# Optimization experiments

Measured on AMD Instinct MI355X. Metric: run time of the kernel, lower is better.

## Reference

```python
import jax, jax.numpy as jnp
import numpy as np

WIN_H, WIN_W = 4, 7
WIN = WIN_H * WIN_W  # 28 sample points == feature channels
GRID_OFF = (0.0, 40.0)
SPATIAL_SCALE = 1.0 / 0.4
BN_EPS = 1e-3


def setup_inputs() -> dict:
    key = jax.random.key(0)
    ks = jax.random.split(key, 5)
    B, Cin, H, W = 4, 256, 200, 176
    Cout, N = WIN, 2048
    x = jax.random.normal(ks[0], (B, Cin, H, W), dtype=jnp.float32)
    # boxes [x, y, z, w, l, h, r] in realistic KITTI ranges
    lo = jnp.array([0.0, -40.0, -3.0, 1.5, 3.2, 1.4, -np.pi], jnp.float32)
    hi = jnp.array([70.0, 40.0, 1.0, 2.0, 4.2, 1.8, np.pi], jnp.float32)
    u = jax.random.uniform(ks[1], (B, N, 7), dtype=jnp.float32)
    guided_anchors = lo + u * (hi - lo)
    w1 = jax.random.normal(ks[2], (Cout, Cin, 3, 3), jnp.float32) * 0.02
    gamma = jnp.ones((Cout,), jnp.float32)
    beta = jnp.zeros((Cout,), jnp.float32)
    running_mean = jnp.zeros((Cout,), jnp.float32)
    running_var = jnp.ones((Cout,), jnp.float32)
    w2 = jax.random.normal(ks[3], (Cout, Cout, 1, 1), jnp.float32) * 0.05
    return dict(x=x, guided_anchors=guided_anchors, w1=w1, gamma=gamma,
                beta=beta, running_mean=running_mean, running_var=running_var, w2=w2)


def _convs(x, w1, gamma, beta, mean, var, w2):
    dn = ('NCHW', 'OIHW', 'NCHW')
    y = jax.lax.conv_general_dilated(x, w1, (1, 1), 'SAME', dimension_numbers=dn)
    scale = gamma * jax.lax.rsqrt(var + BN_EPS)
    y = y * scale[:, None, None] + (beta - mean * scale)[:, None, None]  # BN (inference)
    y = jax.nn.relu(y)
    return jax.lax.conv_general_dilated(y, w2, (1, 1), 'SAME', dimension_numbers=dn)


def _gen_sample_grid(box5):
    xg, yg, wg, lg, rg = (box5[:, i] for i in range(5))
    c = jnp.cos(rg)[:, None, None]
    s = jnp.sin(rg)[:, None, None]
    xx = (jnp.linspace(-0.5, 0.5, WIN_H)[None, :] * wg[:, None])[:, :, None]  # (N,4,1)
    yy = (jnp.linspace(-0.5, 0.5, WIN_W)[None, :] * lg[:, None])[:, None, :]  # (N,1,7)
    xpix = xx * c + yy * s + xg[:, None, None]  # (N,4,7)
    ypix = yy * c - xx * s + yg[:, None, None]  # (N,4,7)
    xs = ((jnp.transpose(xpix, (1, 2, 0)) + GRID_OFF[0]) * SPATIAL_SCALE).reshape(WIN, -1)
    ys = ((jnp.transpose(ypix, (1, 2, 0)) + GRID_OFF[1]) * SPATIAL_SCALE).reshape(WIN, -1)
    return xs, ys


def _bilinear_sample(img, xs, ys):
    # img: (C,H,W); xs, ys: (C,N) pixel coords (align_corners=True semantics,
    # zero padding outside) -> (C,N). Channel c samples at grid row c.
    C, H, W = img.shape
    x0 = jnp.floor(xs); y0 = jnp.floor(ys)
    wx = xs - x0; wy = ys - y0
    cidx = jnp.arange(C)[:, None]

    def gather(yf, xf):
        yi = yf.astype(jnp.int32); xi = xf.astype(jnp.int32)
        valid = (yf >= 0) & (yf <= H - 1) & (xf >= 0) & (xf <= W - 1)
        v = img[cidx, jnp.clip(yi, 0, H - 1), jnp.clip(xi, 0, W - 1)]
        return jnp.where(valid, v, 0.0)

    return (gather(y0, x0) * (1 - wx) * (1 - wy)
            + gather(y0, x0 + 1) * wx * (1 - wy)
            + gather(y0 + 1, x0) * (1 - wx) * wy
            + gather(y0 + 1, x0 + 1) * wx * wy)


def reference(x, guided_anchors, w1, gamma, beta, running_mean, running_var, w2):
    feat = _convs(x, w1, gamma, beta, running_mean, running_var, w2)  # (B,28,H,W)
    box5 = guided_anchors[:, :, jnp.array([0, 1, 3, 4, 6])]           # (B,N,5)
    xs, ys = jax.vmap(_gen_sample_grid)(box5)                          # (B,28,N) each
    vals = jax.vmap(_bilinear_sample)(feat, xs, ys)                    # (B,28,N)
    scores = jnp.mean(vals, axis=1)                                    # (B,N)
    return scores.reshape(-1)                                          # (B*N,)
```

## Files before the change

kernel.cpp:

```cpp
#include <hip/hip_runtime.h>
#include <hip/hip_bf16.h>

#define HH 200
#define WW 176
#define CIN 256
#define CO 28
#define BN_EPS 1e-3f

typedef __attribute__((ext_vector_type(8))) short short8;
typedef __attribute__((ext_vector_type(4))) float f32x4;

static __device__ __forceinline__ ushort f2bf(float f) {
    __hip_bfloat16 h = __float2bfloat16(f);
    return __builtin_bit_cast(ushort, h);
}

__global__ void prep_k(const float* __restrict__ w1, const float* __restrict__ gamma,
                       const float* __restrict__ beta, const float* __restrict__ mean,
                       const float* __restrict__ var, ushort* __restrict__ w1b,
                       float* __restrict__ shift)
{
    int idx = blockIdx.x * 256 + threadIdx.x;
    if (idx < CO) {
        float sc = gamma[idx] * rsqrtf(var[idx] + BN_EPS);
        shift[idx] = beta[idx] - mean[idx] * sc;
    }
    if (idx < 9 * 8 * 2 * 64 * 8) {
        int j  = idx & 7;
        int l  = (idx >> 3) & 63;
        int n  = (idx >> 9) & 1;
        int h  = (idx >> 10) & 7;
        int t  = idx >> 13;
        int co = n * 16 + (l & 15);
        int ci = h * 32 + (l >> 4) * 8 + j;
        float v = 0.f;
        if (co < CO) {
            float sc = gamma[co] * rsqrtf(var[co] + BN_EPS);
            v = w1[(co * CIN + ci) * 9 + t] * sc;
        }
        w1b[idx] = f2bf(v);
    }
}

__global__ __launch_bounds__(256, 4) void conv_mfma_k(
    const float* __restrict__ x, const ushort* __restrict__ w1b,
    const float* __restrict__ shift, float* __restrict__ y1)
{
    __shared__ uint4 sbuf[2][180 * 4];

    const int tid  = threadIdx.x;
    const int lane = tid & 63;
    const int w    = tid >> 6;

    const int NB = 11 * 25 * 4;
    const int q = NB / 8, r = NB % 8;
    const int bid  = blockIdx.x;
    const int xcd  = bid & 7;
    const int rank = bid >> 3;
    const int tile = (xcd < r ? xcd * (q + 1) : r * (q + 1) + (xcd - r) * q) + rank;

    const int tx  = tile % 11;
    const int rem = tile / 11;
    const int ty  = rem % 25;
    const int b   = rem / 25;
    const int x0  = tx * 16, y0 = ty * 8;

    const float* xb = x + (size_t)b * CIN * HH * WW;

    int  soff[3]; bool sval[3]; bool sp[3];
#pragma unroll
    for (int it = 0; it < 3; ++it) {
        int p = it * 64 + lane;
        sp[it] = p < 180;
        int rr = p / 18, cc = p - rr * 18;
        int gy = y0 + rr - 1, gx = x0 + cc - 1;
        bool v = (gy >= 0) & (gy < HH) & (gx >= 0) & (gx < WW) & sp[it];
        sval[it] = v;
        soff[it] = v ? gy * WW + gx : 0;
    }

    float pre[3][8];

    auto issue = [&](int h) {
        const float* pl = xb + (size_t)(h * 32 + w * 8) * (HH * WW);
#pragma unroll
        for (int it = 0; it < 3; ++it) {
            if (sp[it]) {
#pragma unroll
                for (int j = 0; j < 8; ++j)
                    pre[it][j] = pl[(size_t)j * (HH * WW) + soff[it]];
            }
        }
    };

    auto wr = [&](int h) {
#pragma unroll
        for (int it = 0; it < 3; ++it) {
            if (sp[it]) {
                int p = it * 64 + lane;
                ushort u[8];
#pragma unroll
                for (int j = 0; j < 8; ++j)
                    u[j] = sval[it] ? f2bf(pre[it][j]) : (ushort)0;
                uint4 val;
                val.x = (uint)u[0] | ((uint)u[1] << 16);
                val.y = (uint)u[2] | ((uint)u[3] << 16);
                val.z = (uint)u[4] | ((uint)u[5] << 16);
                val.w = (uint)u[6] | ((uint)u[7] << 16);
                sbuf[h & 1][p * 4 + ((w + p) & 3)] = val;
            }
        }
    };

    f32x4 acc[2][2];
#pragma unroll
    for (int m = 0; m < 2; ++m)
#pragma unroll
        for (int n = 0; n < 2; ++n)
            acc[m][n] = (f32x4){0.f, 0.f, 0.f, 0.f};

    auto compute = [&](int h) {
        const uint4* sb = sbuf[h & 1];
#pragma unroll
        for (int t = 0; t < 9; ++t) {
            const int dy = t / 3 - 1, dx = t % 3 - 1;
            short8 bfr[2];
#pragma unroll
            for (int n = 0; n < 2; ++n)
                bfr[n] = *(const short8*)(w1b + (size_t)(((t * 8 + h) * 2 + n) * 64 + lane) * 8);
#pragma unroll
            for (int m = 0; m < 2; ++m) {
                int p = (2 * w + m + dy + 1) * 18 + (lane & 15) + dx + 1;
                uint4 av = sb[p * 4 + (((lane >> 4) + p) & 3)];
                short8 af = __builtin_bit_cast(short8, av);
                acc[m][0] = __builtin_amdgcn_mfma_f32_16x16x32_bf16(af, bfr[0], acc[m][0], 0, 0, 0);
                acc[m][1] = __builtin_amdgcn_mfma_f32_16x16x32_bf16(af, bfr[1], acc[m][1], 0, 0, 0);
            }
        }
    };

    issue(0);
    wr(0);
    __syncthreads();

#pragma unroll 1
    for (int h = 0; h < 7; ++h) {
        issue(h + 1);
        compute(h);
        wr(h + 1);
        __syncthreads();
    }
    compute(7);

    const int co0 = lane & 15;
    const int co1 = 16 + co0;
    const float s0 = shift[co0];
    const float s1 = (co1 < CO) ? shift[co1] : 0.f;
#pragma unroll
    for (int m = 0; m < 2; ++m) {
        int gy = y0 + 2 * w + m;
#pragma unroll
        for (int reg = 0; reg < 4; ++reg) {
            int gx = x0 + (lane >> 4) * 4 + reg;
            float* yp = y1 + ((size_t)(b * HH + gy) * WW + gx) * CO;
            float v0 = acc[m][0][reg] + s0;
            yp[co0] = v0 > 0.f ? v0 : 0.f;
            if (co1 < CO) {
                float v1 = acc[m][1][reg] + s1;
                yp[co1] = v1 > 0.f ? v1 : 0.f;
            }
        }
    }
}

__global__ __launch_bounds__(224) void sample_k(
    const float* __restrict__ y1, const float* __restrict__ ga,
    const float* __restrict__ w2, float* __restrict__ out)
{
    __shared__ float red[224];
    const int lb  = threadIdx.x / CO;
    const int k   = threadIdx.x % CO;
    const int box = blockIdx.x * 8 + lb;
    const int b   = box >> 11;

    const float* ap = ga + (size_t)box * 7;
    float xg = ap[0], yg = ap[1], wg = ap[3], lg = ap[4], rg = ap[6];
    float c = cosf(rg), s = sinf(rg);

    const int i = k / 7, j = k % 7;
    float xx = ((float)i * (1.f / 3.f) - 0.5f) * wg;
    float yy = ((float)j * (1.f / 6.f) - 0.5f) * lg;
    float xs = (xx * c + yy * s + xg) * 2.5f;
    float ys = (yy * c - xx * s + yg + 40.f) * 2.5f;

    float x0 = floorf(xs), y0 = floorf(ys);
    float wx = xs - x0,    wy = ys - y0;

    float w2r[CO];
    const float* w2p = w2 + k * CO;
#pragma unroll
    for (int q = 0; q < 7; ++q) {
        float4 t = ((const float4*)w2p)[q];
        w2r[4*q] = t.x; w2r[4*q+1] = t.y; w2r[4*q+2] = t.z; w2r[4*q+3] = t.w;
    }

    float val = 0.f;
    const float* yb = y1 + (size_t)b * HH * WW * CO;
#pragma unroll
    for (int cor = 0; cor < 4; ++cor) {
        float yf = y0 + (float)(cor >> 1);
        float xf = x0 + (float)(cor & 1);
        float cw = ((cor & 1) ? wx : 1.f - wx) * ((cor >> 1) ? wy : 1.f - wy);
        if (yf >= 0.f && yf <= (float)(HH - 1) && xf >= 0.f && xf <= (float)(WW - 1)) {
            int yi = (int)yf, xi = (int)xf;
            const float* p = yb + ((size_t)yi * WW + xi) * CO;
            float d = 0.f;
#pragma unroll
            for (int q = 0; q < 7; ++q) {
                float4 t = ((const float4*)p)[q];
                d = fmaf(w2r[4*q],   t.x, d);
                d = fmaf(w2r[4*q+1], t.y, d);
                d = fmaf(w2r[4*q+2], t.z, d);
                d = fmaf(w2r[4*q+3], t.w, d);
            }
            val = fmaf(cw, d, val);
        }
    }

    red[threadIdx.x] = val;
    __syncthreads();
    if (k == 0) {
        float sum = 0.f;
#pragma unroll
        for (int q = 0; q < CO; ++q) sum += red[lb * CO + q];
        out[box] = sum * (1.f / 28.f);
    }
}

extern "C" void kernel_launch(void* const* d_in, const int* in_sizes, int n_in,
                              void* d_out, int out_size, void* d_ws, size_t ws_size,
                              hipStream_t stream) {
    const float* x     = (const float*)d_in[0];
    const float* ga    = (const float*)d_in[1];
    const float* w1    = (const float*)d_in[2];
    const float* gamma = (const float*)d_in[3];
    const float* beta  = (const float*)d_in[4];
    const float* mean  = (const float*)d_in[5];
    const float* var   = (const float*)d_in[6];
    const float* w2    = (const float*)d_in[7];
    float* out = (float*)d_out;

    ushort* w1b   = (ushort*)d_ws;
    float*  shift = (float*)((char*)d_ws + 147456);
    float*  y1    = (float*)((char*)d_ws + 147968);

    prep_k<<<(9 * 8 * 2 * 64 * 8 + 255) / 256, 256, 0, stream>>>(
        w1, gamma, beta, mean, var, w1b, shift);

    conv_mfma_k<<<11 * 25 * 4, 256, 0, stream>>>(x, w1b, shift, y1);

    sample_k<<<(4 * 2048) / 8, 224, 0, stream>>>(y1, ga, w2, out);
}
```

Baseline: 89.08 us.

## Stage conv weights into LDS via async global_load_lds and single-buffer input tile

Reorders the prepped bf16 weights so each 32-channel chunk is contiguous, then streams each chunk into a double-buffered LDS array with direct global-to-LDS loads instead of reading the B fragments from global memory inside the MFMA loop. To fit the added 36KB of LDS, the input tile becomes single-buffered, which needs an extra barrier per chunk, and the launch-bounds occupancy hint drops from 4 to 3 blocks. The intent is to replace repeated global weight fetches with LDS reads and overlap the weight prefetch with compute, at the cost of more synchronisation and lower occupancy.

After: 76.26 us. -14.4%, faster.

```diff
diff --git a/kernel.cpp b/kernel.cpp
--- a/kernel.cpp
+++ b/kernel.cpp
@@ -14,6 +14,11 @@
     __hip_bfloat16 h = __float2bfloat16(f);
     return __builtin_bit_cast(ushort, h);
 }
+
+#define GLL16(g, l)                                                         \
+    __builtin_amdgcn_global_load_lds(                                       \
+        (const __attribute__((address_space(1))) void*)(g),                 \
+        (__attribute__((address_space(3))) void*)(l), 16, 0, 0)
 
 __global__ void prep_k(const float* __restrict__ w1, const float* __restrict__ gamma,
                        const float* __restrict__ beta, const float* __restrict__ mean,
@@ -25,12 +30,13 @@
         float sc = gamma[idx] * rsqrtf(var[idx] + BN_EPS);
         shift[idx] = beta[idx] - mean[idx] * sc;
     }
-    if (idx < 9 * 8 * 2 * 64 * 8) {
-        int j  = idx & 7;
-        int l  = (idx >> 3) & 63;
-        int n  = (idx >> 9) & 1;
-        int h  = (idx >> 10) & 7;
-        int t  = idx >> 13;
+    if (idx < 8 * 9 * 2 * 64 * 8) {
+        int j   = idx & 7;
+        int l   = (idx >> 3) & 63;
+        int n   = (idx >> 9) & 1;
+        int rem = idx >> 10;
+        int t   = rem % 9;
+        int h   = rem / 9;
         int co = n * 16 + (l & 15);
         int ci = h * 32 + (l >> 4) * 8 + j;
         float v = 0.f;
@@ -42,11 +48,12 @@
     }
 }
 
-__global__ __launch_bounds__(256, 4) void conv_mfma_k(
+__global__ __launch_bounds__(256, 3) void conv_mfma_k(
     const float* __restrict__ x, const ushort* __restrict__ w1b,
     const float* __restrict__ shift, float* __restrict__ y1)
 {
-    __shared__ uint4 sbuf[2][180 * 4];
+    __shared__ uint4  sbuf[180 * 4];
+    __shared__ ushort wls[2][9216];
 
     const int tid  = threadIdx.x;
     const int lane = tid & 63;
@@ -81,7 +88,7 @@
 
     float pre[3][8];
 
-    auto issue = [&](int h) {
+    auto issue_x = [&](int h) {
         const float* pl = xb + (size_t)(h * 32 + w * 8) * (HH * WW);
 #pragma unroll
         for (int it = 0; it < 3; ++it) {
@@ -93,7 +100,7 @@
         }
     };
 
-    auto wr = [&](int h) {
+    auto wr_x = [&]() {
 #pragma unroll
         for (int it = 0; it < 3; ++it) {
             if (sp[it]) {
@@ -107,8 +114,18 @@
                 val.y = (uint)u[2] | ((uint)u[3] << 16);
                 val.z = (uint)u[4] | ((uint)u[5] << 16);
                 val.w = (uint)u[6] | ((uint)u[7] << 16);
-                sbuf[h & 1][p * 4 + ((w + p) & 3)] = val;
-            }
+                sbuf[p * 4 + ((w + p) & 3)] = val;
+            }
+        }
+    };
+
+    auto gll_w = [&](int h) {
+        const ushort* src = w1b + (size_t)h * 9216;
+#pragma unroll
+        for (int it = 0; it < 5; ++it) {
+            int slot = it * 256 + w * 64;
+            if (slot < 1152)
+                GLL16(src + (size_t)(slot + lane) * 8, &wls[h & 1][slot * 8]);
         }
     };
 
@@ -120,18 +137,18 @@
             acc[m][n] = (f32x4){0.f, 0.f, 0.f, 0.f};
 
     auto compute = [&](int h) {
-        const uint4* sb = sbuf[h & 1];
+        const ushort* wp = wls[h & 1];
 #pragma unroll
         for (int t = 0; t < 9; ++t) {
             const int dy = t / 3 - 1, dx = t % 3 - 1;
             short8 bfr[2];
 #pragma unroll
             for (int n = 0; n < 2; ++n)
-                bfr[n] = *(const short8*)(w1b + (size_t)(((t * 8 + h) * 2 + n) * 64 + lane) * 8);
+                bfr[n] = *(const short8*)&wp[(size_t)((t * 2 + n) * 64 + lane) * 8];
 #pragma unroll
             for (int m = 0; m < 2; ++m) {
                 int p = (2 * w + m + dy + 1) * 18 + (lane & 15) + dx + 1;
-                uint4 av = sb[p * 4 + (((lane >> 4) + p) & 3)];
+                uint4 av = sbuf[p * 4 + (((lane >> 4) + p) & 3)];
                 short8 af = __builtin_bit_cast(short8, av);
                 acc[m][0] = __builtin_amdgcn_mfma_f32_16x16x32_bf16(af, bfr[0], acc[m][0], 0, 0, 0);
                 acc[m][1] = __builtin_amdgcn_mfma_f32_16x16x32_bf16(af, bfr[1], acc[m][1], 0, 0, 0);
@@ -139,18 +156,24 @@
         }
     };
 
-    issue(0);
-    wr(0);
+    gll_w(0);
+    issue_x(0);
+    wr_x();
     __syncthreads();
 
 #pragma unroll 1
-    for (int h = 0; h < 7; ++h) {
-        issue(h + 1);
+    for (int h = 0; h < 8; ++h) {
+        if (h < 7) {
+            gll_w(h + 1);
+            issue_x(h + 1);
+        }
         compute(h);
-        wr(h + 1);
-        __syncthreads();
-    }
-    compute(7);
+        if (h < 7) {
+            __syncthreads();
+            wr_x();
+            __syncthreads();
+        }
+    }
 
     const int co0 = lane & 15;
     const int co1 = 16 + co0;
@@ -254,7 +277,7 @@
     float*  shift = (float*)((char*)d_ws + 147456);
     float*  y1    = (float*)((char*)d_ws + 147968);
 
-    prep_k<<<(9 * 8 * 2 * 64 * 8 + 255) / 256, 256, 0, stream>>>(
+    prep_k<<<(8 * 9 * 2 * 64 * 8 + 255) / 256, 256, 0, stream>>>(
         w1, gamma, beta, mean, var, w1b, shift);
 
     conv_mfma_k<<<11 * 25 * 4, 256, 0, stream>>>(x, w1b, shift, y1);
```
